# Kernel optimization log

Hardware: AMD Instinct MI355X
Metric: run time of the kernel (lower is better)

The kernel has to match this reference:

```python
import jax, jax.numpy as jnp
import numpy as np

N_POINTS = 1_000_000
NUM_PILLARS = 30_000
BN_EPS = 1e-3


def _bn(x, gamma, beta, mean, var):
    # eval-mode BatchNorm1d with eps=0.001
    return (x - mean) * (gamma * jax.lax.rsqrt(var + BN_EPS)) + beta


def setup_inputs() -> dict:
    key = jax.random.key(0)
    ks = jax.random.split(key, 5)
    C1, C2 = 32, 64
    return {
        "points": jax.random.normal(ks[0], (N_POINTS, 5), dtype=jnp.float32),
        "f_center": jax.random.normal(ks[1], (N_POINTS, 3), dtype=jnp.float32),
        "unq_inv": jax.random.randint(ks[2], (N_POINTS,), 0, NUM_PILLARS, dtype=jnp.int32),
        "W1": jax.random.normal(ks[3], (7, C1), dtype=jnp.float32) * 0.1,
        "g1": jnp.ones((C1,), jnp.float32),
        "b1": jnp.zeros((C1,), jnp.float32),
        "m1": jnp.zeros((C1,), jnp.float32),
        "v1": jnp.ones((C1,), jnp.float32),
        "W2": jax.random.normal(ks[4], (C2, C1), dtype=jnp.float32) * 0.1,
        "g2": jnp.ones((C1,), jnp.float32),
        "b2": jnp.zeros((C1,), jnp.float32),
        "m2": jnp.zeros((C1,), jnp.float32),
        "v2": jnp.ones((C1,), jnp.float32),
    }


def reference(points, f_center, unq_inv, W1, g1, b1, m1, v1, W2, g2, b2, m2, v2):
    # gen_feat: concat(f_center, points[:,1:]) -> Linear(no bias) -> BN -> ReLU
    feats = jnp.concatenate([f_center, points[:, 1:]], axis=-1)  # [N, 7]
    h = jnp.maximum(_bn(feats @ W1, g1, b1, m1, v1), 0.0)        # [N, 32]

    # scatter_mean over pillars, then gather back and concat
    seg_sum = jax.ops.segment_sum(h, unq_inv, num_segments=NUM_PILLARS)
    counts = jax.ops.segment_sum(jnp.ones((h.shape[0],), h.dtype), unq_inv,
                                 num_segments=NUM_PILLARS)
    seg_mean = seg_sum / jnp.maximum(counts, 1.0)[:, None]       # [P, 32]
    h2 = jnp.concatenate([h, seg_mean[unq_inv]], axis=1)         # [N, 64]

    # AVFEO: Linear(64,32,no bias) -> BN -> ReLU
    out_fc = jnp.maximum(_bn(h2 @ W2, g2, b2, m2, v2), 0.0)      # [N, 32]

    # scatter_max over pillars (empty pillars -> 0, as torch_scatter)
    seg_max = jax.ops.segment_max(out_fc, unq_inv, num_segments=NUM_PILLARS)
    return jnp.where(jnp.isfinite(seg_max), seg_max, 0.0)        # [P, 32]
```

## Files before the change

### kernel.cpp

```cpp
#include <hip/hip_runtime.h>

typedef __attribute__((ext_vector_type(8))) short short8;
typedef __attribute__((ext_vector_type(4))) float floatx4;

static constexpr float EPS = 1e-3f;

#define CAP 96
#define CSTRIDE 32

#define P_W1F  0
#define P_B1F  224
#define P_W2L  256
#define P_B2F  1280
#define P_W2UT 1312
#define PREP_F 2048

__device__ __forceinline__ unsigned short f2bf(float x) {
  unsigned u = __float_as_uint(x);
  u += 0x7FFFu + ((u >> 16) & 1u);
  return (unsigned short)(u >> 16);
}

__global__ __launch_bounds__(256)
void k_prep(const float* __restrict__ W1, const float* __restrict__ g1,
            const float* __restrict__ b1, const float* __restrict__ m1,
            const float* __restrict__ v1,
            const float* __restrict__ W2, const float* __restrict__ g2,
            const float* __restrict__ b2, const float* __restrict__ m2,
            const float* __restrict__ v2, float* __restrict__ prep) {
  int t = threadIdx.x;
  for (int i = t; i < 224; i += 256) {
    int c = i & 31;
    prep[P_W1F + i] = W1[i] * (g1[c] * rsqrtf(v1[c] + EPS));
  }
  if (t < 32) {
    float s1 = g1[t] * rsqrtf(v1[t] + EPS);
    float s2 = g2[t] * rsqrtf(v2[t] + EPS);
    prep[P_B1F + t] = b1[t] - m1[t] * s1;
    prep[P_B2F + t] = b2[t] - m2[t] * s2;
  }
  unsigned short* wt = (unsigned short*)(prep + P_W2UT);
  for (int i = t; i < 1024; i += 256) {
    int k = i >> 5, c = i & 31;
    float s2 = g2[c] * rsqrtf(v2[c] + EPS);
    prep[P_W2L + i] = W2[(32 + k) * 32 + c] * s2;
    wt[c * 32 + k] = f2bf(W2[k * 32 + c] * s2);
  }
}

__global__ __launch_bounds__(256)
void k_build_feat(const float* __restrict__ points, const float* __restrict__ fc,
                  const int* __restrict__ unq, int* __restrict__ cnt,
                  float* __restrict__ feat, int N) {
  int i = blockIdx.x * 256 + threadIdx.x;
  if (i >= N) return;
  int p = unq[i];
  float4 a, b;
  a.x = fc[3 * i];         a.y = fc[3 * i + 1];     a.z = fc[3 * i + 2];
  a.w = points[5 * i + 1];
  b.x = points[5 * i + 2]; b.y = points[5 * i + 3]; b.z = points[5 * i + 4];
  b.w = 0.f;
  int slot = atomicAdd(&cnt[p * CSTRIDE], 1);
  if (slot < CAP) {
    float4* dst = (float4*)(feat + ((size_t)p * CAP + slot) * 8);
    dst[0] = a;
    dst[1] = b;
  }
}

__global__ __launch_bounds__(256)
void k_pillar(const float* __restrict__ prep, const int* __restrict__ cnt,
              const float* __restrict__ feat, float* __restrict__ out,
              int npil) {
  __shared__ __align__(16) float fbuf[4][CAP * 8];
  __shared__ __align__(16) unsigned short hbuf[4][CAP * 32];
  __shared__ __align__(16) unsigned short w2t[1024];
  __shared__ float sumb[4][32];

  const int t = threadIdx.x, w = t >> 6, lane = t & 63;

  ((uint2*)w2t)[t] = ((const uint2*)(prep + P_W2UT))[t];
  __syncthreads();

  const int p = blockIdx.x * 4 + w;
  if (p >= npil) return;
  int n = cnt[p * CSTRIDE];
  n = n < CAP ? n : CAP;

  const int c = lane & 31, half = lane >> 5;

  const floatx4* src4 = (const floatx4*)(feat + (size_t)p * CAP * 8);
  floatx4* f4 = (floatx4*)fbuf[w];
  for (int q = lane; q < 2 * n; q += 64) f4[q] = src4[q];
  __builtin_amdgcn_wave_barrier();

  float w1c[7];
#pragma unroll
  for (int r = 0; r < 7; ++r) w1c[r] = prep[P_W1F + r * 32 + c];
  const float b1c = prep[P_B1F + c];
  const float b2c = prep[P_B2F + c];

  float ps = 0.f;
  for (int j = half; j < n; j += 2) {
    const float* f = fbuf[w] + j * 8;
    floatx4 fa = *(const floatx4*)f, fb = *(const floatx4*)(f + 4);
    float d = fa.x * w1c[0];
    d = fmaf(fa.y, w1c[1], d);
    d = fmaf(fa.z, w1c[2], d);
    d = fmaf(fa.w, w1c[3], d);
    d = fmaf(fb.x, w1c[4], d);
    d = fmaf(fb.y, w1c[5], d);
    d = fmaf(fb.z, w1c[6], d);
    float h = fmaxf(d + b1c, 0.f);
    ps += h;
    hbuf[w][j * 32 + c] = f2bf(h);
  }
  ps += __shfl_xor(ps, 32);
  if (half == 0) sumb[w][c] = ps;
  __builtin_amdgcn_wave_barrier();

  float acc = 0.f;
  const floatx4* sb4 = (const floatx4*)sumb[w];
#pragma unroll
  for (int kq = 0; kq < 8; ++kq) {
    floatx4 sv = sb4[kq];
    acc = fmaf(sv.x, prep[P_W2L + (kq * 4 + 0) * 32 + c], acc);
    acc = fmaf(sv.y, prep[P_W2L + (kq * 4 + 1) * 32 + c], acc);
    acc = fmaf(sv.z, prep[P_W2L + (kq * 4 + 2) * 32 + c], acc);
    acc = fmaf(sv.w, prep[P_W2L + (kq * 4 + 3) * 32 + c], acc);
  }
  const float inv_n = (n > 0) ? 1.f / (float)n : 1.f;
  const float pc = fmaf(inv_n, acc, b2c);

  const int m16 = lane & 15, q4 = lane >> 4;
  short8 bf0 = *(const short8*)(w2t + m16 * 32 + q4 * 8);
  short8 bf1 = *(const short8*)(w2t + (m16 + 16) * 32 + q4 * 8);
  float m0 = -INFINITY, m1 = -INFINITY;
  const int ntiles = (n + 15) >> 4;
  for (int rt = 0; rt < ntiles; ++rt) {
    short8 af = *(const short8*)(hbuf[w] + (rt * 16 + m16) * 32 + q4 * 8);
    floatx4 z = {0.f, 0.f, 0.f, 0.f};
    floatx4 a0 = __builtin_amdgcn_mfma_f32_16x16x32_bf16(af, bf0, z, 0, 0, 0);
    floatx4 a1 = __builtin_amdgcn_mfma_f32_16x16x32_bf16(af, bf1, z, 0, 0, 0);
    const int rowb = rt * 16 + q4 * 4;
#pragma unroll
    for (int r = 0; r < 4; ++r) {
      if (rowb + r < n) {
        m0 = fmaxf(m0, a0[r]);
        m1 = fmaxf(m1, a1[r]);
      }
    }
  }
  m0 = fmaxf(m0, __shfl_xor(m0, 16));
  m0 = fmaxf(m0, __shfl_xor(m0, 32));
  m1 = fmaxf(m1, __shfl_xor(m1, 16));
  m1 = fmaxf(m1, __shfl_xor(m1, 32));

  if (lane < 32) {
    float q = (lane & 16) ? m1 : m0;
    out[p * 32 + lane] = fmaxf(q + pc, 0.f);
  }
}

extern "C" void kernel_launch(void* const* d_in, const int* in_sizes, int n_in,
                              void* d_out, int out_size, void* d_ws, size_t ws_size,
                              hipStream_t stream) {
  const float* points = (const float*)d_in[0];
  const float* fc     = (const float*)d_in[1];
  const int*   unq    = (const int*)d_in[2];
  const float* W1 = (const float*)d_in[3];
  const float* g1 = (const float*)d_in[4];
  const float* b1 = (const float*)d_in[5];
  const float* m1 = (const float*)d_in[6];
  const float* v1 = (const float*)d_in[7];
  const float* W2 = (const float*)d_in[8];
  const float* g2 = (const float*)d_in[9];
  const float* b2 = (const float*)d_in[10];
  const float* m2 = (const float*)d_in[11];
  const float* v2 = (const float*)d_in[12];

  const int N    = in_sizes[0] / 5;
  const int NPIL = out_size / 32;

  float* ws = (float*)d_ws;
  int* cnt = (int*)ws;
  const size_t cnt_f  = ((size_t)NPIL * CSTRIDE + 255) & ~(size_t)255;
  float* prep = ws + cnt_f;
  float* feat = prep + PREP_F;

  hipMemsetAsync(cnt, 0, (size_t)NPIL * CSTRIDE * sizeof(int), stream);

  k_prep<<<1, 256, 0, stream>>>(W1, g1, b1, m1, v1, W2, g2, b2, m2, v2, prep);

  const int nb = (N + 255) / 256;
  k_build_feat<<<nb, 256, 0, stream>>>(points, fc, unq, cnt, feat, N);

  const int nbp = (NPIL + 3) / 4;
  k_pillar<<<nbp, 256, 0, stream>>>(prep, cnt, feat, (float*)d_out, NPIL);
}
```

Before: 186.7 us.

## Pack point features as fp16 and batch four points per thread in scatter

Each point's seven input features are now stored as a packed 16-byte fp16 row instead of 32 bytes of fp32, halving the scatter buffer's write and read traffic. The build kernel handles four points per thread so several atomics and loads are in flight at once. The pillar kernel reads rows straight from global memory instead of staging them in LDS. The features are rounded to fp16 before the first linear layer, which adds some precision loss.

```diff
diff --git a/kernel.cpp b/kernel.cpp
--- a/kernel.cpp
+++ b/kernel.cpp
@@ -1,4 +1,5 @@
 #include <hip/hip_runtime.h>
+#include <hip/hip_fp16.h>
 
 typedef __attribute__((ext_vector_type(8))) short short8;
 typedef __attribute__((ext_vector_type(4))) float floatx4;
@@ -19,6 +20,14 @@
   unsigned u = __float_as_uint(x);
   u += 0x7FFFu + ((u >> 16) & 1u);
   return (unsigned short)(u >> 16);
+}
+__device__ __forceinline__ unsigned pack2h(float a, float b) {
+  __half2 h = __floats2half2_rn(a, b);
+  return *reinterpret_cast<unsigned*>(&h);
+}
+__device__ __forceinline__ float2 unp2h(unsigned u) {
+  __half2 h = *reinterpret_cast<__half2*>(&u);
+  return __half22float2(h);
 }
 
 __global__ __launch_bounds__(256)
@@ -51,28 +60,40 @@
 __global__ __launch_bounds__(256)
 void k_build_feat(const float* __restrict__ points, const float* __restrict__ fc,
                   const int* __restrict__ unq, int* __restrict__ cnt,
-                  float* __restrict__ feat, int N) {
-  int i = blockIdx.x * 256 + threadIdx.x;
-  if (i >= N) return;
-  int p = unq[i];
-  float4 a, b;
-  a.x = fc[3 * i];         a.y = fc[3 * i + 1];     a.z = fc[3 * i + 2];
-  a.w = points[5 * i + 1];
-  b.x = points[5 * i + 2]; b.y = points[5 * i + 3]; b.z = points[5 * i + 4];
-  b.w = 0.f;
-  int slot = atomicAdd(&cnt[p * CSTRIDE], 1);
-  if (slot < CAP) {
-    float4* dst = (float4*)(feat + ((size_t)p * CAP + slot) * 8);
-    dst[0] = a;
-    dst[1] = b;
-  }
+                  uint4* __restrict__ feat, int N) {
+  const int base = blockIdx.x * 1024 + threadIdx.x;
+  int  pp[4];
+  uint4 row[4];
+  bool val[4];
+#pragma unroll
+  for (int u = 0; u < 4; ++u) {
+    int i = base + u * 256;
+    val[u] = (i < N);
+    if (val[u]) {
+      pp[u] = unq[i];
+      float f0 = fc[3 * i], f1 = fc[3 * i + 1], f2 = fc[3 * i + 2];
+      float f3 = points[5 * i + 1], f4 = points[5 * i + 2];
+      float f5 = points[5 * i + 3], f6 = points[5 * i + 4];
+      row[u].x = pack2h(f0, f1);
+      row[u].y = pack2h(f2, f3);
+      row[u].z = pack2h(f4, f5);
+      row[u].w = pack2h(f6, 0.f);
+    }
+  }
+  int slot[4];
+#pragma unroll
+  for (int u = 0; u < 4; ++u)
+    if (val[u]) slot[u] = atomicAdd(&cnt[pp[u] * CSTRIDE], 1);
+#pragma unroll
+  for (int u = 0; u < 4; ++u)
+    if (val[u] && slot[u] < CAP)
+      feat[(size_t)pp[u] * CAP + slot[u]] = row[u];
 }
 
 __global__ __launch_bounds__(256)
 void k_pillar(const float* __restrict__ prep, const int* __restrict__ cnt,
-              const float* __restrict__ feat, float* __restrict__ out,
+              const uint4* __restrict__ feat, float* __restrict__ out,
               int npil) {
-  __shared__ __align__(16) float fbuf[4][CAP * 8];
   __shared__ __align__(16) unsigned short hbuf[4][CAP * 32];
   __shared__ __align__(16) unsigned short w2t[1024];
   __shared__ float sumb[4][32];
@@ -89,28 +110,25 @@
 
   const int c = lane & 31, half = lane >> 5;
 
-  const floatx4* src4 = (const floatx4*)(feat + (size_t)p * CAP * 8);
-  floatx4* f4 = (floatx4*)fbuf[w];
-  for (int q = lane; q < 2 * n; q += 64) f4[q] = src4[q];
-  __builtin_amdgcn_wave_barrier();
-
   float w1c[7];
 #pragma unroll
   for (int r = 0; r < 7; ++r) w1c[r] = prep[P_W1F + r * 32 + c];
   const float b1c = prep[P_B1F + c];
   const float b2c = prep[P_B2F + c];
 
+  const uint4* __restrict__ rows = feat + (size_t)p * CAP;
   float ps = 0.f;
   for (int j = half; j < n; j += 2) {
-    const float* f = fbuf[w] + j * 8;
-    floatx4 fa = *(const floatx4*)f, fb = *(const floatx4*)(f + 4);
-    float d = fa.x * w1c[0];
-    d = fmaf(fa.y, w1c[1], d);
-    d = fmaf(fa.z, w1c[2], d);
-    d = fmaf(fa.w, w1c[3], d);
-    d = fmaf(fb.x, w1c[4], d);
-    d = fmaf(fb.y, w1c[5], d);
-    d = fmaf(fb.z, w1c[6], d);
+    uint4 rv = rows[j];
+    float2 f01 = unp2h(rv.x), f23 = unp2h(rv.y);
+    float2 f45 = unp2h(rv.z), f6x = unp2h(rv.w);
+    float d = f01.x * w1c[0];
+    d = fmaf(f01.y, w1c[1], d);
+    d = fmaf(f23.x, w1c[2], d);
+    d = fmaf(f23.y, w1c[3], d);
+    d = fmaf(f45.x, w1c[4], d);
+    d = fmaf(f45.y, w1c[5], d);
+    d = fmaf(f6x.x, w1c[6], d);
     float h = fmaxf(d + b1c, 0.f);
     ps += h;
     hbuf[w][j * 32 + c] = f2bf(h);
@@ -184,15 +202,15 @@
 
   float* ws = (float*)d_ws;
   int* cnt = (int*)ws;
-  const size_t cnt_f  = ((size_t)NPIL * CSTRIDE + 255) & ~(size_t)255;
+  const size_t cnt_f = ((size_t)NPIL * CSTRIDE + 255) & ~(size_t)255;
   float* prep = ws + cnt_f;
-  float* feat = prep + PREP_F;
+  uint4* feat = (uint4*)(prep + PREP_F);
 
   hipMemsetAsync(cnt, 0, (size_t)NPIL * CSTRIDE * sizeof(int), stream);
 
   k_prep<<<1, 256, 0, stream>>>(W1, g1, b1, m1, v1, W2, g2, b2, m2, v2, prep);
 
-  const int nb = (N + 255) / 256;
+  const int nb = (N + 1023) / 1024;
   k_build_feat<<<nb, 256, 0, stream>>>(points, fc, unq, cnt, feat, N);
 
   const int nbp = (NPIL + 3) / 4;
```

Result: slower. 208.3 us (+11.6%).
